# Kernel tuning notes

Hardware: AMD Instinct MI355X
Metric: run time of the kernel (lower is better)

## Reference

```python
import jax, jax.numpy as jnp
import numpy as np

L = 2          # num_layers
H = 1024       # hidden_size
XD = 192       # exogenous feature dim
YD = 64        # out_size == y dim
IN = XD + YD   # lstm input size
B = 256
PRE_LEN = 64
FWD_LEN = 48


def setup_inputs() -> dict:
    key = jax.random.key(0)
    ks = jax.random.split(key, 16)
    s = 0.05  # keep gate pre-activations in a sane range
    inp = {
        "pre_x": jax.random.normal(ks[0], (PRE_LEN, B, XD), jnp.float32),
        "pre_y": jax.random.normal(ks[1], (PRE_LEN, B, YD), jnp.float32),
        "forward_x": jax.random.normal(ks[2], (FWD_LEN, B, XD), jnp.float32),
        # layer 0 LSTM params (torch layout: w_ih (4H, IN), w_hh (4H, H))
        "w_ih_0": jax.random.normal(ks[3], (4 * H, IN), jnp.float32) * s,
        "w_hh_0": jax.random.normal(ks[4], (4 * H, H), jnp.float32) * s,
        "b_ih_0": jax.random.normal(ks[5], (4 * H,), jnp.float32) * s,
        "b_hh_0": jax.random.normal(ks[6], (4 * H,), jnp.float32) * s,
        # layer 1
        "w_ih_1": jax.random.normal(ks[7], (4 * H, H), jnp.float32) * s,
        "w_hh_1": jax.random.normal(ks[8], (4 * H, H), jnp.float32) * s,
        "b_ih_1": jax.random.normal(ks[9], (4 * H,), jnp.float32) * s,
        "b_hh_1": jax.random.normal(ks[10], (4 * H,), jnp.float32) * s,
        # fc: Linear(H,H) -> Tanh -> Linear(H,YD)
        "fc_w1": jax.random.normal(ks[11], (H, H), jnp.float32) * s,
        "fc_b1": jax.random.normal(ks[12], (H,), jnp.float32) * s,
        "fc_w2": jax.random.normal(ks[13], (YD, H), jnp.float32) * s,
        "fc_b2": jax.random.normal(ks[14], (YD,), jnp.float32) * s,
    }
    return inp


def _lstm_cell(x, h, c, w_ih, w_hh, b_ih, b_hh):
    # torch gate order: i, f, g, o
    z = x @ w_ih.T + h @ w_hh.T + (b_ih + b_hh)  # (B, 4H)
    i, f, g, o = jnp.split(z, 4, axis=-1)
    c_new = jax.nn.sigmoid(f) * c + jax.nn.sigmoid(i) * jnp.tanh(g)
    h_new = jax.nn.sigmoid(o) * jnp.tanh(c_new)
    return h_new, c_new


def _stack_step(layers, x_t, hs, cs):
    # layers: list of (w_ih, w_hh, b_ih, b_hh); hs, cs: (L, B, H)
    new_h, new_c = [], []
    inp = x_t
    for l, (w_ih, w_hh, b_ih, b_hh) in enumerate(layers):
        h, c = _lstm_cell(inp, hs[l], cs[l], w_ih, w_hh, b_ih, b_hh)
        new_h.append(h)
        new_c.append(c)
        inp = h
    return jnp.stack(new_h), jnp.stack(new_c), inp  # inp = top-layer output


def reference(pre_x, pre_y, forward_x,
              w_ih_0, w_hh_0, b_ih_0, b_hh_0,
              w_ih_1, w_hh_1, b_ih_1, b_hh_1,
              fc_w1, fc_b1, fc_w2, fc_b2):
    layers = [(w_ih_0, w_hh_0, b_ih_0, b_hh_0),
              (w_ih_1, w_hh_1, b_ih_1, b_hh_1)]

    def fc(x):
        return jnp.tanh(x @ fc_w1.T + fc_b1) @ fc_w2.T + fc_b2

    batch = pre_x.shape[1]
    hs0 = jnp.zeros((L, batch, H), pre_x.dtype)
    cs0 = jnp.zeros((L, batch, H), pre_x.dtype)

    # --- warmup encode over concat(pre_x, pre_y) ---
    xy = jnp.concatenate([pre_x, pre_y], axis=2)  # (PRE_LEN, B, IN)

    def enc_step(carry, x_t):
        hs, cs = carry
        hs, cs, top = _stack_step(layers, x_t, hs, cs)
        return (hs, cs), top

    (hs, cs), enc_outs = jax.lax.scan(enc_step, (hs0, cs0), xy)
    top = enc_outs[-1]          # output[-1] from the encoding pass
    last_y = pre_y[-1]

    def dec_step(carry, fx_t):
        hs, cs, top, last_y = carry
        est = fc(top) + last_y                        # (B, YD)
        x_in = jnp.concatenate([fx_t, est], axis=1)   # (B, IN)
        hs, cs, top = _stack_step(layers, x_in, hs, cs)
        return (hs, cs, top, est), est

    _, est_all = jax.lax.scan(dec_step, (hs, cs, top, last_y), forward_x)
    return est_all  # (FWD_LEN, B, YD)
```

## Files before the change

kernel.cpp:

```cpp
#include <hip/hip_runtime.h>
#include <stdint.h>

typedef unsigned short u16;
typedef __attribute__((ext_vector_type(8))) _Float16 f16x8;
typedef __attribute__((ext_vector_type(4))) float f32x4;

__device__ inline f16x8 ldfrag(const u16* p) { return *(const f16x8*)p; }

__device__ __forceinline__ f16x8 ldfrag_dc(const u16* p) {
    f16x8 r;
    asm volatile("global_load_dwordx4 %0, %1, off sc1" : "=&v"(r) : "v"(p));
    return r;
}
__device__ __forceinline__ void st_u16_dc(u16* p, u16 v) {
    unsigned vv = v;
    asm volatile("global_store_short %0, %1, off sc1" :: "v"(p), "v"(vv) : "memory");
}
__device__ __forceinline__ void wait_vm0() {
    asm volatile("s_waitcnt vmcnt(0)" ::: "memory");
    __builtin_amdgcn_sched_barrier(0);
}

__device__ inline u16 f2h(float x) {
    _Float16 h = (_Float16)x;
    union { _Float16 h; u16 u; } v; v.h = h;
    return v.u;
}
__device__ inline float sigmoidf_(float x) { return 1.0f / (1.0f + expf(-x)); }

__device__ __forceinline__ void gbar(unsigned* cnt, unsigned* rel, unsigned ep) {
    __syncthreads();
    if (threadIdx.x == 0) {
        unsigned old = __hip_atomic_fetch_add(cnt, 1u, __ATOMIC_RELAXED,
                                              __HIP_MEMORY_SCOPE_AGENT);
        if (old == ep * 256u + 255u) {
            __hip_atomic_store(rel, ep + 1u, __ATOMIC_RELAXED,
                               __HIP_MEMORY_SCOPE_AGENT);
        } else {
            unsigned r;
            do {
                __builtin_amdgcn_s_sleep(8);
                r = __hip_atomic_load(rel, __ATOMIC_RELAXED,
                                      __HIP_MEMORY_SCOPE_AGENT);
            } while (r < ep + 1u);
        }
    }
    __syncthreads();
    asm volatile("" ::: "memory");
}


struct PP {
    const u16* xyenc;
    u16* xdec;
    const u16 *wih0, *whh0, *wih1, *whh1, *fcw1, *fcw2;
    const float *b0s, *b1s, *fcb1, *fcb2, *pre_y;
    u16 *h0a, *h0b, *h1a, *h1b, *ufc;
    float* out;
    unsigned *cnt, *rel;
};

static __device__ __forceinline__ void lstm_phase(
    const u16* __restrict__ AFa, int KBa, bool adyn, const u16* __restrict__ BFa,
    const u16* __restrict__ AFh, const u16* __restrict__ BFh,
    const float* __restrict__ bsum, float* creg, u16* __restrict__ h_out,
    int ct, int mg, int w, int lane, f32x4 (*red)[16][64])
{
    const int l15  = lane & 15;
    const int quad = lane >> 4;

    f32x4 acc[4][4];
    #pragma unroll
    for (int t = 0; t < 4; ++t)
        #pragma unroll
        for (int g = 0; g < 4; ++g) acc[t][g] = (f32x4){0, 0, 0, 0};

    {
        const int q = KBa >> 3;
        for (int kb = w * q; kb < w * q + q; ++kb) {
            f16x8 a[4], b[4];
            if (adyn) {
                #pragma unroll
                for (int t = 0; t < 4; ++t)
                    a[t] = ldfrag_dc(AFa + (((size_t)(mg * 4 + t) * KBa + kb) * 64 + lane) * 8);
            } else {
                #pragma unroll
                for (int t = 0; t < 4; ++t)
                    a[t] = ldfrag(AFa + (((size_t)(mg * 4 + t) * KBa + kb) * 64 + lane) * 8);
            }
            #pragma unroll
            for (int g = 0; g < 4; ++g)
                b[g] = ldfrag(BFa + (((size_t)(ct * 4 + g) * KBa + kb) * 64 + lane) * 8);
            wait_vm0();
            #pragma unroll
            for (int t = 0; t < 4; ++t)
                #pragma unroll
                for (int g = 0; g < 4; ++g)
                    acc[t][g] = __builtin_amdgcn_mfma_f32_16x16x32_f16(a[t], b[g], acc[t][g], 0, 0, 0);
        }
    }
    {
        #pragma unroll 2
        for (int kb = w * 4; kb < w * 4 + 4; ++kb) {
            f16x8 a[4], b[4];
            #pragma unroll
            for (int t = 0; t < 4; ++t)
                a[t] = ldfrag_dc(AFh + (((size_t)(mg * 4 + t) * 32 + kb) * 64 + lane) * 8);
            #pragma unroll
            for (int g = 0; g < 4; ++g)
                b[g] = ldfrag(BFh + (((size_t)(ct * 4 + g) * 32 + kb) * 64 + lane) * 8);
            wait_vm0();
            #pragma unroll
            for (int t = 0; t < 4; ++t)
                #pragma unroll
                for (int g = 0; g < 4; ++g)
                    acc[t][g] = __builtin_amdgcn_mfma_f32_16x16x32_f16(a[t], b[g], acc[t][g], 0, 0, 0);
        }
    }

    if (w >= 4) {
        #pragma unroll
        for (int t = 0; t < 4; ++t)
            #pragma unroll
            for (int g = 0; g < 4; ++g)
                red[w - 4][t * 4 + g][lane] = acc[t][g];
    }
    __syncthreads();
    if (w < 4) {
        #pragma unroll
        for (int t = 0; t < 4; ++t)
            #pragma unroll
            for (int g = 0; g < 4; ++g)
                red[w][t * 4 + g][lane] += acc[t][g];
    }
    __syncthreads();
    if (w < 4) {
        f32x4 z[4];
        #pragma unroll
        for (int g = 0; g < 4; ++g)
            z[g] = red[0][w * 4 + g][lane] + red[1][w * 4 + g][lane] +
                   red[2][w * 4 + g][lane] + red[3][w * 4 + g][lane];

        const int col   = ct * 16 + l15;
        const int mtile = mg * 4 + w;
        float bv[4];
        #pragma unroll
        for (int g = 0; g < 4; ++g) bv[g] = bsum[g * 1024 + col];
        const int hkb = col >> 5, hquad = (col >> 3) & 3, hj = col & 7;
        #pragma unroll
        for (int r = 0; r < 4; ++r) {
            const int rl = quad * 4 + r;
            const float zi = z[0][r] + bv[0];
            const float zf = z[1][r] + bv[1];
            const float zg = z[2][r] + bv[2];
            const float zo = z[3][r] + bv[3];
            const float cv = creg[r];
            const float cn = sigmoidf_(zf) * cv + sigmoidf_(zi) * tanhf(zg);
            creg[r] = cn;
            st_u16_dc(h_out + (((size_t)mtile * 32 + hkb) * 64 + hquad * 16 + rl) * 8 + hj,
                      f2h(sigmoidf_(zo) * tanhf(cn)));
        }
    }
}

static __device__ __forceinline__ void fc1_phase(
    const u16* __restrict__ AFx, const u16* __restrict__ BFw,
    const float* __restrict__ bias, u16* __restrict__ U,
    int b, int w, int lane, f32x4 (*red)[16][64])
{
    const int mt = b >> 4, ctq = b & 15;
    const int l15 = lane & 15, quad = lane >> 4;
    f32x4 acc[4];
    #pragma unroll
    for (int g = 0; g < 4; ++g) acc[g] = (f32x4){0, 0, 0, 0};

    #pragma unroll
    for (int k = 0; k < 4; ++k) {
        const int kb = w * 4 + k;
        f16x8 a = ldfrag_dc(AFx + (((size_t)mt * 32 + kb) * 64 + lane) * 8);
        f16x8 bb[4];
        #pragma unroll
        for (int g = 0; g < 4; ++g)
            bb[g] = ldfrag(BFw + (((size_t)(ctq * 4 + g) * 32 + kb) * 64 + lane) * 8);
        wait_vm0();
        #pragma unroll
        for (int g = 0; g < 4; ++g)
            acc[g] = __builtin_amdgcn_mfma_f32_16x16x32_f16(a, bb[g], acc[g], 0, 0, 0);
    }

    f32x4 (*r8)[4][64] = (f32x4 (*)[4][64])red;
    #pragma unroll
    for (int g = 0; g < 4; ++g) r8[w][g][lane] = acc[g];
    __syncthreads();
    if (w < 4) {
        f32x4 z = r8[0][w][lane];
        #pragma unroll
        for (int p = 1; p < 8; ++p) z += r8[p][w][lane];
        const int col = ctq * 64 + w * 16 + l15;
        const float bv = bias[col];
        const int ukb = col >> 5, uq = (col >> 3) & 3, uj = col & 7;
        #pragma unroll
        for (int r = 0; r < 4; ++r) {
            const int rl = quad * 4 + r;
            st_u16_dc(U + (((size_t)mt * 32 + ukb) * 64 + uq * 16 + rl) * 8 + uj,
                      f2h(tanhf(z[r] + bv)));
        }
    }
}

static __device__ __forceinline__ void fc2_phase(
    const u16* __restrict__ AFu, const u16* __restrict__ BFw2,
    const float* __restrict__ b2, float* estreg,
    float* __restrict__ out_t, u16* __restrict__ xdec_t,
    int b, int w, int lane, f32x4 (*red)[16][64])
{
    f32x4 (*rr)[64] = (f32x4 (*)[64])red;
    const int l15 = lane & 15, quad = lane >> 4;
    const int mt = b >> 2, cg = b & 3;
    if (b < 64) {
        f32x4 acc = (f32x4){0, 0, 0, 0};
        #pragma unroll
        for (int k = 0; k < 4; ++k) {
            const int kb = w * 4 + k;
            f16x8 a = ldfrag_dc(AFu + (((size_t)mt * 32 + kb) * 64 + lane) * 8);
            f16x8 bb = ldfrag(BFw2 + (((size_t)cg * 32 + kb) * 64 + lane) * 8);
            wait_vm0();
            acc = __builtin_amdgcn_mfma_f32_16x16x32_f16(a, bb, acc, 0, 0, 0);
        }
        rr[w][lane] = acc;
    }
    __syncthreads();
    if (b < 64 && w == 0) {
        f32x4 acc = rr[0][lane];
        #pragma unroll
        for (int p = 1; p < 8; ++p) acc += rr[p][lane];
        const int col = cg * 16 + l15;
        const float bv = b2[col];
        const int cx = 192 + col;
        const int xkb = cx >> 5, xq = (cx >> 3) & 3, xj = cx & 7;
        #pragma unroll
        for (int r = 0; r < 4; ++r) {
            const int rl = quad * 4 + r;
            const int row = mt * 16 + rl;
            const float v = acc[r] + bv + estreg[r];
            estreg[r] = v;
            out_t[row * 64 + col] = v;
            st_u16_dc(xdec_t + (((size_t)mt * 8 + xkb) * 64 + xq * 16 + rl) * 8 + xj, f2h(v));
        }
    }
}

__global__ __launch_bounds__(512, 2) void persist_k(PP p)
{
    __shared__ f32x4 red[4][16][64];

    const int tid  = threadIdx.x;
    const int w    = tid >> 6;
    const int lane = tid & 63;
    const int l15  = lane & 15;
    const int quad = lane >> 4;
    const int b    = blockIdx.x;
    const int ct   = b & 63;
    const int mg   = b >> 6;

    unsigned ep = 0;

    float c0reg[4] = {0.f, 0.f, 0.f, 0.f};
    float c1reg[4] = {0.f, 0.f, 0.f, 0.f};
    float estreg[4] = {0.f, 0.f, 0.f, 0.f};
    if (b < 64) {
        const int fmt = b >> 2, fcg = b & 3;
        #pragma unroll
        for (int r = 0; r < 4; ++r) {
            const int row = fmt * 16 + quad * 4 + r;
            const int col = fcg * 16 + l15;
            estreg[r] = p.pre_y[(size_t)63 * 16384 + row * 64 + col];
        }
    }

    u16 *h0c = p.h0a, *h0n = p.h0b;
    u16 *h1c = p.h1a, *h1n = p.h1b;

    for (int t = 0; t < 64; ++t) {
        lstm_phase(p.xyenc + (size_t)t * 65536, 8, false, p.wih0, h0c, p.whh0,
                   p.b0s, c0reg, h0n, ct, mg, w, lane, red);
        gbar(p.cnt, p.rel, ep); ++ep;
        lstm_phase(h0n, 32, true, p.wih1, h1c, p.whh1,
                   p.b1s, c1reg, h1n, ct, mg, w, lane, red);
        gbar(p.cnt, p.rel, ep); ++ep;
        u16* tmp;
        tmp = h0c; h0c = h0n; h0n = tmp;
        tmp = h1c; h1c = h1n; h1n = tmp;
    }

    for (int t = 0; t < 48; ++t) {
        fc1_phase(h1c, p.fcw1, p.fcb1, p.ufc, b, w, lane, red);
        gbar(p.cnt, p.rel, ep); ++ep;
        fc2_phase(p.ufc, p.fcw2, p.fcb2, estreg,
                  p.out + (size_t)t * 16384, p.xdec + (size_t)t * 65536,
                  b, w, lane, red);
        gbar(p.cnt, p.rel, ep); ++ep;
        if (t < 47) {
            lstm_phase(p.xdec + (size_t)t * 65536, 8, true, p.wih0, h0c, p.whh0,
                       p.b0s, c0reg, h0n, ct, mg, w, lane, red);
            gbar(p.cnt, p.rel, ep); ++ep;
            lstm_phase(h0n, 32, true, p.wih1, h1c, p.whh1,
                       p.b1s, c1reg, h1n, ct, mg, w, lane, red);
            gbar(p.cnt, p.rel, ep); ++ep;
            u16* tmp;
            tmp = h0c; h0c = h0n; h0n = tmp;
            tmp = h1c; h1c = h1n; h1n = tmp;
        }
    }
}

__global__ void cvt_bfrag_k(const float* __restrict__ src, u16* __restrict__ dst,
                            int K, int kbshift, int S1, int S2, int total) {
    int i = blockIdx.x * 256 + threadIdx.x;
    if (i >= total) return;
    const int lane = i & 63;
    const int kb   = (i >> 6) & ((1 << kbshift) - 1);
    const int rest = i >> (6 + kbshift);
    const int sub  = rest & 3;
    const int grp  = rest >> 2;
    const int row  = sub * S1 + grp * S2 + (lane & 15);
    const int colK = kb * 32 + (lane >> 4) * 8;
    const float* s = src + (size_t)row * K + colK;
    u16* d = dst + (size_t)i * 8;
    #pragma unroll
    for (int j = 0; j < 8; ++j) d[j] = f2h(s[j]);
}
__global__ void bias_k(const float* __restrict__ a, const float* __restrict__ b,
                       float* __restrict__ d, int n) {
    int i = blockIdx.x * 256 + threadIdx.x;
    if (i < n) d[i] = a[i] + b[i];
}
__global__ void zeroh_k(u16* h0, u16* h1, unsigned* bar) {
    int i = blockIdx.x * 256 + threadIdx.x;
    h0[i] = 0; h1[i] = 0;
    if (i < 128) bar[i] = 0u;
}
__global__ void pack_enc_k(const float* __restrict__ pre_x, const float* __restrict__ pre_y,
                           u16* __restrict__ xy) {
    int i = blockIdx.x * 256 + threadIdx.x;
    const int lane  = i & 63;
    const int kb    = (i >> 6) & 7;
    const int mtile = (i >> 9) & 15;
    const int t     = i >> 13;
    const int row   = mtile * 16 + (lane & 15);
    const int cb    = kb * 32 + (lane >> 4) * 8;
    u16* d = xy + (size_t)i * 8;
    #pragma unroll
    for (int j = 0; j < 8; ++j) {
        const int col = cb + j;
        const float v = (col < 192) ? pre_x[((size_t)t * 256 + row) * 192 + col]
                                    : pre_y[((size_t)t * 256 + row) * 64 + (col - 192)];
        d[j] = f2h(v);
    }
}
__global__ void pack_dec_k(const float* __restrict__ fx, u16* __restrict__ xd,
                           int total_threads) {
    int i = blockIdx.x * 256 + threadIdx.x;
    if (i >= total_threads) return;
    const int lane  = i & 63;
    int rest = i >> 6;
    const int kb    = rest % 6;  rest /= 6;
    const int mtile = rest & 15;
    const int t     = rest >> 4;
    const int row   = mtile * 16 + (lane & 15);
    const int cb    = kb * 32 + (lane >> 4) * 8;
    u16* d = xd + ((((size_t)t * 16 + mtile) * 8 + kb) * 64 + lane) * 8;
    #pragma unroll
    for (int j = 0; j < 8; ++j)
        d[j] = f2h(fx[((size_t)t * 256 + row) * 192 + cb + j]);
}

extern "C" void kernel_launch(void* const* d_in, const int* in_sizes, int n_in,
                              void* d_out, int out_size, void* d_ws, size_t ws_size,
                              hipStream_t stream) {
    const float* pre_x  = (const float*)d_in[0];
    const float* pre_y  = (const float*)d_in[1];
    const float* fx     = (const float*)d_in[2];
    const float* w_ih_0 = (const float*)d_in[3];
    const float* w_hh_0 = (const float*)d_in[4];
    const float* b_ih_0 = (const float*)d_in[5];
    const float* b_hh_0 = (const float*)d_in[6];
    const float* w_ih_1 = (const float*)d_in[7];
    const float* w_hh_1 = (const float*)d_in[8];
    const float* b_ih_1 = (const float*)d_in[9];
    const float* b_hh_1 = (const float*)d_in[10];
    const float* fc_w1  = (const float*)d_in[11];
    const float* fc_b1  = (const float*)d_in[12];
    const float* fc_w2  = (const float*)d_in[13];
    const float* fc_b2  = (const float*)d_in[14];

    size_t off = 0;
    char* wsb = (char*)d_ws;
    auto alloc = [&](size_t bytes) -> void* {
        void* p = wsb + off;
        off += (bytes + 255) & ~(size_t)255;
        return p;
    };
    u16* wih0 = (u16*)alloc((size_t)4096 * 256 * 2);
    u16* whh0 = (u16*)alloc((size_t)4096 * 1024 * 2);
    u16* wih1 = (u16*)alloc((size_t)4096 * 1024 * 2);
    u16* whh1 = (u16*)alloc((size_t)4096 * 1024 * 2);
    u16* fcw1 = (u16*)alloc((size_t)1024 * 1024 * 2);
    u16* fcw2 = (u16*)alloc((size_t)64 * 1024 * 2);
    float* b0s = (float*)alloc(4096 * 4);
    float* b1s = (float*)alloc(4096 * 4);
    u16* xyenc = (u16*)alloc((size_t)64 * 256 * 256 * 2);
    u16* xdec  = (u16*)alloc((size_t)48 * 256 * 256 * 2);
    u16* h0a = (u16*)alloc((size_t)256 * 1024 * 2);
    u16* h0b = (u16*)alloc((size_t)256 * 1024 * 2);
    u16* h1a = (u16*)alloc((size_t)256 * 1024 * 2);
    u16* h1b = (u16*)alloc((size_t)256 * 1024 * 2);
    u16* ufc = (u16*)alloc((size_t)256 * 1024 * 2);
    unsigned* bar = (unsigned*)alloc(512);

    cvt_bfrag_k<<<512, 256, 0, stream>>>(w_ih_0, wih0, 256, 3, 1024, 16, 64 * 4 * 8 * 64);
    cvt_bfrag_k<<<2048, 256, 0, stream>>>(w_hh_0, whh0, 1024, 5, 1024, 16, 64 * 4 * 32 * 64);
    cvt_bfrag_k<<<2048, 256, 0, stream>>>(w_ih_1, wih1, 1024, 5, 1024, 16, 64 * 4 * 32 * 64);
    cvt_bfrag_k<<<2048, 256, 0, stream>>>(w_hh_1, whh1, 1024, 5, 1024, 16, 64 * 4 * 32 * 64);
    cvt_bfrag_k<<<512, 256, 0, stream>>>(fc_w1, fcw1, 1024, 5, 16, 64, 16 * 4 * 32 * 64);
    cvt_bfrag_k<<<32, 256, 0, stream>>>(fc_w2, fcw2, 1024, 5, 16, 0, 1 * 4 * 32 * 64);
    bias_k<<<16, 256, 0, stream>>>(b_ih_0, b_hh_0, b0s, 4096);
    bias_k<<<16, 256, 0, stream>>>(b_ih_1, b_hh_1, b1s, 4096);
    zeroh_k<<<1024, 256, 0, stream>>>(h0a, h1a, bar);
    pack_enc_k<<<2048, 256, 0, stream>>>(pre_x, pre_y, xyenc);
    pack_dec_k<<<1152, 256, 0, stream>>>(fx, xdec, 48 * 16 * 6 * 64);

    PP p;
    p.xyenc = xyenc; p.xdec = xdec;
    p.wih0 = wih0; p.whh0 = whh0; p.wih1 = wih1; p.whh1 = whh1;
    p.fcw1 = fcw1; p.fcw2 = fcw2;
    p.b0s = b0s; p.b1s = b1s; p.fcb1 = fc_b1; p.fcb2 = fc_b2; p.pre_y = pre_y;
    p.h0a = h0a; p.h0b = h0b; p.h1a = h1a; p.h1b = h1b; p.ufc = ufc;
    p.out = (float*)d_out;
    p.cnt = bar; p.rel = bar + 64;

    void* args[] = { &p };
    hipLaunchCooperativeKernel((const void*)persist_k, dim3(256), dim3(512),
                               args, 0, stream);
}
```

Measured before the change: 3.861 ms.

## Use per-timestep ring buffers for hidden states so plain cached loads are safe

Replaces the ping-pong hidden-state and fc buffers with rings that hold one slot per timestep, so no address is ever rewritten during the kernel. Because each slot is written only once, stale non-coherent cache lines cannot be hit, and the cache-bypassing sc1 loads and explicit vmcnt(0) waits are replaced by ordinary loads the compiler can schedule and pipeline. It also unrolls the input-projection loop. This costs far more workspace memory and relies on the cache not holding stale lines for addresses that were never read before they were written.

```diff
diff --git a/kernel.cpp b/kernel.cpp
--- a/kernel.cpp
+++ b/kernel.cpp
@@ -6,21 +6,10 @@
 typedef __attribute__((ext_vector_type(4))) float f32x4;
 
 __device__ inline f16x8 ldfrag(const u16* p) { return *(const f16x8*)p; }
-
-__device__ __forceinline__ f16x8 ldfrag_dc(const u16* p) {
-    f16x8 r;
-    asm volatile("global_load_dwordx4 %0, %1, off sc1" : "=&v"(r) : "v"(p));
-    return r;
-}
 __device__ __forceinline__ void st_u16_dc(u16* p, u16 v) {
     unsigned vv = v;
     asm volatile("global_store_short %0, %1, off sc1" :: "v"(p), "v"(vv) : "memory");
 }
-__device__ __forceinline__ void wait_vm0() {
-    asm volatile("s_waitcnt vmcnt(0)" ::: "memory");
-    __builtin_amdgcn_sched_barrier(0);
-}
-
 __device__ inline u16 f2h(float x) {
     _Float16 h = (_Float16)x;
     union { _Float16 h; u16 u; } v; v.h = h;
@@ -55,13 +44,14 @@
     u16* xdec;
     const u16 *wih0, *whh0, *wih1, *whh1, *fcw1, *fcw2;
     const float *b0s, *b1s, *fcb1, *fcb2, *pre_y;
-    u16 *h0a, *h0b, *h1a, *h1b, *ufc;
+    const u16 *h0init, *h1init;
+    u16 *h0ring, *h1ring, *ufcring;
     float* out;
     unsigned *cnt, *rel;
 };
 
 static __device__ __forceinline__ void lstm_phase(
-    const u16* __restrict__ AFa, int KBa, bool adyn, const u16* __restrict__ BFa,
+    const u16* __restrict__ AFa, int KBa, const u16* __restrict__ BFa,
     const u16* __restrict__ AFh, const u16* __restrict__ BFh,
     const float* __restrict__ bsum, float* creg, u16* __restrict__ h_out,
     int ct, int mg, int w, int lane, f32x4 (*red)[16][64])
@@ -77,21 +67,15 @@
 
     {
         const int q = KBa >> 3;
+        #pragma unroll 2
         for (int kb = w * q; kb < w * q + q; ++kb) {
             f16x8 a[4], b[4];
-            if (adyn) {
-                #pragma unroll
-                for (int t = 0; t < 4; ++t)
-                    a[t] = ldfrag_dc(AFa + (((size_t)(mg * 4 + t) * KBa + kb) * 64 + lane) * 8);
-            } else {
-                #pragma unroll
-                for (int t = 0; t < 4; ++t)
-                    a[t] = ldfrag(AFa + (((size_t)(mg * 4 + t) * KBa + kb) * 64 + lane) * 8);
-            }
+            #pragma unroll
+            for (int t = 0; t < 4; ++t)
+                a[t] = ldfrag(AFa + (((size_t)(mg * 4 + t) * KBa + kb) * 64 + lane) * 8);
             #pragma unroll
             for (int g = 0; g < 4; ++g)
                 b[g] = ldfrag(BFa + (((size_t)(ct * 4 + g) * KBa + kb) * 64 + lane) * 8);
-            wait_vm0();
             #pragma unroll
             for (int t = 0; t < 4; ++t)
                 #pragma unroll
@@ -105,11 +89,10 @@
             f16x8 a[4], b[4];
             #pragma unroll
             for (int t = 0; t < 4; ++t)
-                a[t] = ldfrag_dc(AFh + (((size_t)(mg * 4 + t) * 32 + kb) * 64 + lane) * 8);
+                a[t] = ldfrag(AFh + (((size_t)(mg * 4 + t) * 32 + kb) * 64 + lane) * 8);
             #pragma unroll
             for (int g = 0; g < 4; ++g)
                 b[g] = ldfrag(BFh + (((size_t)(ct * 4 + g) * 32 + kb) * 64 + lane) * 8);
-            wait_vm0();
             #pragma unroll
             for (int t = 0; t < 4; ++t)
                 #pragma unroll
@@ -177,15 +160,12 @@
     #pragma unroll
     for (int k = 0; k < 4; ++k) {
         const int kb = w * 4 + k;
-        f16x8 a = ldfrag_dc(AFx + (((size_t)mt * 32 + kb) * 64 + lane) * 8);
-        f16x8 bb[4];
-        #pragma unroll
-        for (int g = 0; g < 4; ++g)
-            bb[g] = ldfrag(BFw + (((size_t)(ctq * 4 + g) * 32 + kb) * 64 + lane) * 8);
-        wait_vm0();
-        #pragma unroll
-        for (int g = 0; g < 4; ++g)
-            acc[g] = __builtin_amdgcn_mfma_f32_16x16x32_f16(a, bb[g], acc[g], 0, 0, 0);
+        f16x8 a = ldfrag(AFx + (((size_t)mt * 32 + kb) * 64 + lane) * 8);
+        #pragma unroll
+        for (int g = 0; g < 4; ++g) {
+            f16x8 bb = ldfrag(BFw + (((size_t)(ctq * 4 + g) * 32 + kb) * 64 + lane) * 8);
+            acc[g] = __builtin_amdgcn_mfma_f32_16x16x32_f16(a, bb, acc[g], 0, 0, 0);
+        }
     }
 
     f32x4 (*r8)[4][64] = (f32x4 (*)[4][64])red;
@@ -222,9 +202,8 @@
         #pragma unroll
         for (int k = 0; k < 4; ++k) {
             const int kb = w * 4 + k;
-            f16x8 a = ldfrag_dc(AFu + (((size_t)mt * 32 + kb) * 64 + lane) * 8);
+            f16x8 a = ldfrag(AFu + (((size_t)mt * 32 + kb) * 64 + lane) * 8);
             f16x8 bb = ldfrag(BFw2 + (((size_t)cg * 32 + kb) * 64 + lane) * 8);
-            wait_vm0();
             acc = __builtin_amdgcn_mfma_f32_16x16x32_f16(a, bb, acc, 0, 0, 0);
         }
         rr[w][lane] = acc;
@@ -278,38 +257,40 @@
         }
     }
 
-    u16 *h0c = p.h0a, *h0n = p.h0b;
-    u16 *h1c = p.h1a, *h1n = p.h1b;
+    const size_t HS = 262144;
+    const u16* h0prev = p.h0init;
+    const u16* h1prev = p.h1init;
 
     for (int t = 0; t < 64; ++t) {
-        lstm_phase(p.xyenc + (size_t)t * 65536, 8, false, p.wih0, h0c, p.whh0,
-                   p.b0s, c0reg, h0n, ct, mg, w, lane, red);
+        u16* h0cur = p.h0ring + (size_t)t * HS;
+        lstm_phase(p.xyenc + (size_t)t * 65536, 8, p.wih0, h0prev, p.whh0,
+                   p.b0s, c0reg, h0cur, ct, mg, w, lane, red);
         gbar(p.cnt, p.rel, ep); ++ep;
-        lstm_phase(h0n, 32, true, p.wih1, h1c, p.whh1,
-                   p.b1s, c1reg, h1n, ct, mg, w, lane, red);
+        u16* h1cur = p.h1ring + (size_t)t * HS;
+        lstm_phase(h0cur, 32, p.wih1, h1prev, p.whh1,
+                   p.b1s, c1reg, h1cur, ct, mg, w, lane, red);
         gbar(p.cnt, p.rel, ep); ++ep;
-        u16* tmp;
-        tmp = h0c; h0c = h0n; h0n = tmp;
-        tmp = h1c; h1c = h1n; h1n = tmp;
+        h0prev = h0cur; h1prev = h1cur;
     }
 
     for (int t = 0; t < 48; ++t) {
-        fc1_phase(h1c, p.fcw1, p.fcb1, p.ufc, b, w, lane, red);
+        u16* ufct = p.ufcring + (size_t)t * HS;
+        fc1_phase(h1prev, p.fcw1, p.fcb1, ufct, b, w, lane, red);
         gbar(p.cnt, p.rel, ep); ++ep;
-        fc2_phase(p.ufc, p.fcw2, p.fcb2, estreg,
+        fc2_phase(ufct, p.fcw2, p.fcb2, estreg,
                   p.out + (size_t)t * 16384, p.xdec + (size_t)t * 65536,
                   b, w, lane, red);
         gbar(p.cnt, p.rel, ep); ++ep;
         if (t < 47) {
-            lstm_phase(p.xdec + (size_t)t * 65536, 8, true, p.wih0, h0c, p.whh0,
-                       p.b0s, c0reg, h0n, ct, mg, w, lane, red);
+            u16* h0cur = p.h0ring + (size_t)(64 + t) * HS;
+            lstm_phase(p.xdec + (size_t)t * 65536, 8, p.wih0, h0prev, p.whh0,
+                       p.b0s, c0reg, h0cur, ct, mg, w, lane, red);
             gbar(p.cnt, p.rel, ep); ++ep;
-            lstm_phase(h0n, 32, true, p.wih1, h1c, p.whh1,
-                       p.b1s, c1reg, h1n, ct, mg, w, lane, red);
+            u16* h1cur = p.h1ring + (size_t)(64 + t) * HS;
+            lstm_phase(h0cur, 32, p.wih1, h1prev, p.whh1,
+                       p.b1s, c1reg, h1cur, ct, mg, w, lane, red);
             gbar(p.cnt, p.rel, ep); ++ep;
-            u16* tmp;
-            tmp = h0c; h0c = h0n; h0n = tmp;
-            tmp = h1c; h1c = h1n; h1n = tmp;
+            h0prev = h0cur; h1prev = h1cur;
         }
     }
 }
@@ -335,9 +316,9 @@
     int i = blockIdx.x * 256 + threadIdx.x;
     if (i < n) d[i] = a[i] + b[i];
 }
-__global__ void zeroh_k(u16* h0, u16* h1, unsigned* bar) {
+__global__ void zeroh_k(u16* h0i, u16* h1i, unsigned* bar) {
     int i = blockIdx.x * 256 + threadIdx.x;
-    h0[i] = 0; h1[i] = 0;
+    h0i[i] = 0; h1i[i] = 0;
     if (i < 128) bar[i] = 0u;
 }
 __global__ void pack_enc_k(const float* __restrict__ pre_x, const float* __restrict__ pre_y,
@@ -411,11 +392,11 @@
     float* b1s = (float*)alloc(4096 * 4);
     u16* xyenc = (u16*)alloc((size_t)64 * 256 * 256 * 2);
     u16* xdec  = (u16*)alloc((size_t)48 * 256 * 256 * 2);
-    u16* h0a = (u16*)alloc((size_t)256 * 1024 * 2);
-    u16* h0b = (u16*)alloc((size_t)256 * 1024 * 2);
-    u16* h1a = (u16*)alloc((size_t)256 * 1024 * 2);
-    u16* h1b = (u16*)alloc((size_t)256 * 1024 * 2);
-    u16* ufc = (u16*)alloc((size_t)256 * 1024 * 2);
+    u16* h0init = (u16*)alloc((size_t)256 * 1024 * 2);
+    u16* h1init = (u16*)alloc((size_t)256 * 1024 * 2);
+    u16* h0ring = (u16*)alloc((size_t)111 * 256 * 1024 * 2);
+    u16* h1ring = (u16*)alloc((size_t)111 * 256 * 1024 * 2);
+    u16* ufcring = (u16*)alloc((size_t)48 * 256 * 1024 * 2);
     unsigned* bar = (unsigned*)alloc(512);
 
     cvt_bfrag_k<<<512, 256, 0, stream>>>(w_ih_0, wih0, 256, 3, 1024, 16, 64 * 4 * 8 * 64);
@@ -426,7 +407,7 @@
     cvt_bfrag_k<<<32, 256, 0, stream>>>(fc_w2, fcw2, 1024, 5, 16, 0, 1 * 4 * 32 * 64);
     bias_k<<<16, 256, 0, stream>>>(b_ih_0, b_hh_0, b0s, 4096);
     bias_k<<<16, 256, 0, stream>>>(b_ih_1, b_hh_1, b1s, 4096);
-    zeroh_k<<<1024, 256, 0, stream>>>(h0a, h1a, bar);
+    zeroh_k<<<1024, 256, 0, stream>>>(h0init, h1init, bar);
     pack_enc_k<<<2048, 256, 0, stream>>>(pre_x, pre_y, xyenc);
     pack_dec_k<<<1152, 256, 0, stream>>>(fx, xdec, 48 * 16 * 6 * 64);
 
@@ -435,7 +416,8 @@
     p.wih0 = wih0; p.whh0 = whh0; p.wih1 = wih1; p.whh1 = whh1;
     p.fcw1 = fcw1; p.fcw2 = fcw2;
     p.b0s = b0s; p.b1s = b1s; p.fcb1 = fc_b1; p.fcb2 = fc_b2; p.pre_y = pre_y;
-    p.h0a = h0a; p.h0b = h0b; p.h1a = h1a; p.h1b = h1b; p.ufc = ufc;
+    p.h0init = h0init; p.h1init = h1init;
+    p.h0ring = h0ring; p.h1ring = h1ring; p.ufcring = ufcring;
     p.out = (float*)d_out;
     p.cnt = bar; p.rel = bar + 64;
 
```

Measured after the change: 3.741 ms. 1.03x faster.
